# Kernel optimization log

Hardware: AMD Instinct MI355X
Metric: run time of the kernel (lower is better)

The kernel has to match this reference:

```python
import jax, jax.numpy as jnp
import numpy as np

B, S, D_MODEL, H = 2, 2048, 1024, 16
DIMS = D_MODEL // H  # 64


def setup_inputs() -> dict:
    key = jax.random.key(0)
    ks = jax.random.split(key, 7)
    scale = 1.0 / np.sqrt(D_MODEL)
    x = jax.random.normal(ks[0], (B, S, D_MODEL), dtype=jnp.float32)
    # Stacked per-head projection params: nn.Linear(d_model, dims) per head
    Wq = jax.random.uniform(ks[1], (H, DIMS, D_MODEL), minval=-scale, maxval=scale, dtype=jnp.float32)
    Wk = jax.random.uniform(ks[2], (H, DIMS, D_MODEL), minval=-scale, maxval=scale, dtype=jnp.float32)
    Wv = jax.random.uniform(ks[3], (H, DIMS, D_MODEL), minval=-scale, maxval=scale, dtype=jnp.float32)
    bq = jax.random.uniform(ks[4], (H, DIMS), minval=-scale, maxval=scale, dtype=jnp.float32)
    bk = jax.random.uniform(ks[5], (H, DIMS), minval=-scale, maxval=scale, dtype=jnp.float32)
    bv = jax.random.uniform(ks[6], (H, DIMS), minval=-scale, maxval=scale, dtype=jnp.float32)
    return {"x": x, "Wq": Wq, "Wk": Wk, "Wv": Wv, "bq": bq, "bk": bk, "bv": bv}


def reference(x, Wq, Wk, Wv, bq, bk, bv):
    # Per-head linear projections: [B,S,D] x [H,E,D] -> [B,H,S,E]
    q = jnp.einsum('bsd,hed->bhse', x, Wq) + bq[None, :, None, :]
    k = jnp.einsum('bsd,hed->bhse', x, Wk) + bk[None, :, None, :]
    v = jnp.einsum('bsd,hed->bhse', x, Wv) + bv[None, :, None, :]
    norm = DIMS ** (-0.5)
    # (q @ k^T) * norm @ v  -- NO softmax, as in the source
    scores = jnp.einsum('bhse,bhte->bhst', q, k) * norm  # [B,H,S,S]
    out = jnp.einsum('bhst,bhte->bhse', scores, v)       # [B,H,S,E]
    # concat heads along feature dim (head order matches torch.cat)
    return out.transpose(0, 2, 1, 3).reshape(B, S, H * DIMS)
```

## Files before the change

### kernel.cpp

```cpp
#include <hip/hip_runtime.h>


typedef __attribute__((ext_vector_type(8))) __bf16 bf16x8;
typedef __attribute__((ext_vector_type(8))) short short8;
typedef __attribute__((ext_vector_type(4))) float f32x4;
typedef __attribute__((ext_vector_type(4))) unsigned short ushort4v;

#define NX  4194304
#define NW1 1048576
#define NW  3145728

__device__ __forceinline__ float bf2f(unsigned short u) {
  union { unsigned int i; float f; } v; v.i = ((unsigned int)u) << 16; return v.f;
}
__device__ __forceinline__ unsigned short f2bf(float f) {
  union { float f; unsigned int i; } v; v.f = f;
  unsigned int u = v.i;
  u += 0x7fffu + ((u >> 16) & 1u);
  return (unsigned short)(u >> 16);
}

__global__ __launch_bounds__(256) void convert_pack(
    const float* __restrict__ x,
    const float* __restrict__ wq, const float* __restrict__ wk,
    const float* __restrict__ wv,
    const float* __restrict__ bq, const float* __restrict__ bk,
    const float* __restrict__ bv,
    unsigned short* __restrict__ Xbf, unsigned short* __restrict__ Wcat,
    float* __restrict__ Bcat)
{
  const long long t8 = ((long long)blockIdx.x * 256 + threadIdx.x) * 8;
  const float* src;
  unsigned short* dst;
  long long off;
  if (t8 < NX) {
    src = x; dst = Xbf; off = t8;
  } else if (t8 < NX + NW) {
    const long long w = t8 - NX;
    const int z = (int)(w >> 20);
    off = w & (NW1 - 1);
    src = (z == 0) ? wq : (z == 1) ? wk : wv;
    dst = Wcat + (long long)z * NW1;
  } else if (t8 < NX + NW + 3072) {
    const long long bo = t8 - (NX + NW);
    const int z = (int)(bo >> 10);
    const long long o2 = bo & 1023;
    const float* bsrc = (z == 0) ? bq : (z == 1) ? bk : bv;
    *(f32x4*)(Bcat + z * 1024 + o2)     = *(const f32x4*)(bsrc + o2);
    *(f32x4*)(Bcat + z * 1024 + o2 + 4) = *(const f32x4*)(bsrc + o2 + 4);
    return;
  } else {
    return;
  }
  f32x4 v0 = *(const f32x4*)(src + off);
  f32x4 v1 = *(const f32x4*)(src + off + 4);
  union { short8 s; unsigned short u[8]; } o;
#pragma unroll
  for (int j = 0; j < 4; ++j) {
    o.u[j]     = f2bf(v0[j]);
    o.u[4 + j] = f2bf(v1[j]);
  }
  *(short8*)(dst + off) = o.s;
}

#define ABUF_B 16384
#define TILE_B 28672
__global__ __launch_bounds__(512, 2) void qkv_gemm(
    const unsigned short* __restrict__ Xbf,
    const unsigned short* __restrict__ Wcat,
    const float* __restrict__ Bcat,
    unsigned short* __restrict__ Qt,
    unsigned short* __restrict__ Kt,
    unsigned short* __restrict__ Vt)
{
  __shared__ unsigned char lds[3 * TILE_B];

  const int tid = threadIdx.x;
  int bid = blockIdx.x;
  bid = (bid & 7) * 32 + (bid >> 3);
  const int colBase = (bid & 15) * 192;
  const int rowBase = (bid >> 4) * 256;

  const int lane = tid & 63;
  const int wid  = tid >> 6;
  const int wr = (wid >> 2) * 128;
  const int wc = (wid & 3) * 48;
  const int lr = lane & 15;
  const int lk = lane >> 4;
  const int fofs = (lk ^ ((lr >> 1) & 3)) << 4;

  const bool isA = (tid < 256);
  const int nload = isA ? 4 : 3;
  const int tloc = tid & 255;

  const unsigned short* gp[4];
  int lofs[4];
#pragma unroll
  for (int l = 0; l < 4; ++l) {
    const int unit = l * 256 + tloc;
    const int row  = unit >> 2;
    const int sc   = ((unit & 3) ^ ((row >> 1) & 3)) << 3;
    const int rowc = (!isA && row > 191) ? 0 : row;
    gp[l]  = isA ? (Xbf  + (size_t)(rowBase + rowc) * 1024 + sc)
                 : (Wcat + (size_t)(colBase + rowc) * 1024 + sc);
    lofs[l] = (isA ? 0 : ABUF_B) + unit * 16;
  }

  f32x4 acc[8][3] = {};
  short8 stg[3][4];

#pragma unroll
  for (int s = 0; s < 3; ++s)
#pragma unroll
    for (int l = 0; l < 4; ++l)
      if (l < nload) stg[s][l] = *(const short8*)(gp[l] + s * 32);
#pragma unroll
  for (int l = 0; l < 4; ++l)
    if (l < nload) *(short8*)(lds + lofs[l]) = stg[0][l];
  asm volatile("s_waitcnt lgkmcnt(0)" ::: "memory");

#define ITER(J, U, U1)                                                     \
  if ((J) < 32) {                                                          \
    __builtin_amdgcn_s_barrier();                                          \
    __builtin_amdgcn_sched_barrier(0);                                     \
    const unsigned char* Ab_ = lds + (U) * TILE_B;                         \
    const unsigned char* Bb_ = Ab_ + ABUF_B;                               \
    bf16x8 a_[8], b_[3];                                                   \
    _Pragma("unroll") for (int m = 0; m < 8; ++m)                          \
      a_[m] = *(const bf16x8*)(Ab_ + (wr + m * 16 + lr) * 64 + fofs);      \
    _Pragma("unroll") for (int n = 0; n < 3; ++n)                          \
      b_[n] = *(const bf16x8*)(Bb_ + (wc + n * 16 + lr) * 64 + fofs);      \
    if ((J) + 1 < 32) {                                                    \
      unsigned char* Wb_ = lds + (U1) * TILE_B;                            \
      _Pragma("unroll") for (int l = 0; l < 4; ++l)                        \
        if (l < nload) *(short8*)(Wb_ + lofs[l]) = stg[U1][l];             \
    }                                                                      \
    if ((J) + 3 < 32) {                                                    \
      _Pragma("unroll") for (int l = 0; l < 4; ++l)                        \
        if (l < nload) stg[U][l] = *(const short8*)(gp[l] + ((J) + 3) * 32);\
    }                                                                      \
    __builtin_amdgcn_s_setprio(1);                                         \
    _Pragma("unroll") for (int m = 0; m < 8; ++m)                          \
      _Pragma("unroll") for (int n = 0; n < 3; ++n)                        \
        acc[m][n] = __builtin_amdgcn_mfma_f32_16x16x32_bf16(               \
            a_[m], b_[n], acc[m][n], 0, 0, 0);                             \
    __builtin_amdgcn_s_setprio(0);                                         \
    asm volatile("s_waitcnt lgkmcnt(0)" ::: "memory");                     \
  }

  for (int jb = 0; jb < 32; jb += 3) {
    ITER(jb + 0, 0, 1);
    ITER(jb + 1, 1, 2);
    ITER(jb + 2, 2, 0);
  }
#undef ITER

  const int bB = rowBase >> 11;
#pragma unroll
  for (int n = 0; n < 3; ++n) {
    const int colG = colBase + wc + n * 16 + lr;
    const float bval = Bcat[colG];
    const int zone = colG >> 10;
    unsigned short* __restrict__ T = (zone == 0) ? Qt : (zone == 1) ? Kt : Vt;
    const int hf = (colG >> 6) & 15;
    const int f  = colG & 63;
    const size_t rowOff = ((size_t)(bB * 16 + hf) * 64 + f) * 2048;
#pragma unroll
    for (int m = 0; m < 8; ++m) {
      const int t = (rowBase + wr + m * 16 + lk * 4) & 2047;
      ushort4v pk;
#pragma unroll
      for (int jj = 0; jj < 4; ++jj)
        pk[jj] = f2bf(acc[m][n][jj] + bval);
      *(ushort4v*)&T[rowOff + t] = pk;
    }
  }
}

__global__ __launch_bounds__(64) void kv_outer(
    const unsigned short* __restrict__ Kt,
    const unsigned short* __restrict__ Vt,
    float* __restrict__ Mpart)
{
  const int lane = threadIdx.x;
  const int blk = blockIdx.x;
  const int bh = blk >> 3, tc = blk & 7;
  const int lr = lane & 15, lk = lane >> 4;
  const size_t base = (size_t)bh * 64 * 2048;

  f32x4 acc[4][4] = {};
#pragma unroll
  for (int ks = 0; ks < 8; ++ks) {
    const int t0 = tc * 256 + ks * 32 + lk * 8;
    bf16x8 af[4], bf[4];
#pragma unroll
    for (int m = 0; m < 4; ++m)
      af[m] = *(const bf16x8*)&Kt[base + (size_t)(m * 16 + lr) * 2048 + t0];
#pragma unroll
    for (int n = 0; n < 4; ++n)
      bf[n] = *(const bf16x8*)&Vt[base + (size_t)(n * 16 + lr) * 2048 + t0];
#pragma unroll
    for (int m = 0; m < 4; ++m)
#pragma unroll
      for (int n = 0; n < 4; ++n)
        acc[m][n] = __builtin_amdgcn_mfma_f32_16x16x32_bf16(af[m], bf[n], acc[m][n], 0, 0, 0);
  }
  float* out = Mpart + (size_t)blk * 4096;
#pragma unroll
  for (int m = 0; m < 4; ++m)
#pragma unroll
    for (int n = 0; n < 4; ++n)
#pragma unroll
      for (int j = 0; j < 4; ++j)
        out[(m * 16 + lk * 4 + j) * 64 + n * 16 + lr] = acc[m][n][j];
}

__global__ __launch_bounds__(256) void qm_out(
    const unsigned short* __restrict__ Qt, const float* __restrict__ Mpart,
    float* __restrict__ Out)
{
  __shared__ float Ms[64 * 64];
  __shared__ float Qst[64 * 132];
  const int tid = threadIdx.x;
  const int b = blockIdx.z, h = blockIdx.y, s0 = blockIdx.x * 128;
  const int bh = b * 16 + h;

#pragma unroll
  for (int i = 0; i < 4; ++i) {
    const int off = i * 1024 + tid * 4;
    f32x4 s = {};
#pragma unroll
    for (int ch = 0; ch < 8; ++ch)
      s += *(const f32x4*)&Mpart[((size_t)bh * 8 + ch) * 4096 + off];
    s *= 0.125f;
    *(f32x4*)&Ms[off] = s;
  }
  const size_t qbase = (size_t)bh * 64 * 2048;
#pragma unroll
  for (int i = 0; i < 4; ++i) {
    const int slot = i * 256 + tid;
    const int f = slot >> 4, c = slot & 15;
    short8 q = *(const short8*)&Qt[qbase + (size_t)f * 2048 + s0 + c * 8];
#pragma unroll
    for (int j = 0; j < 8; ++j)
      Qst[f * 132 + c * 8 + j] = bf2f((unsigned short)q[j]);
  }
  __syncthreads();

  const int s = (tid >> 3) * 4;
  const int e0 = (tid & 7) * 8;
  float acc2[4][8] = {};
  for (int f = 0; f < 64; ++f) {
    f32x4 m0 = *(const f32x4*)&Ms[f * 64 + e0];
    f32x4 m1 = *(const f32x4*)&Ms[f * 64 + e0 + 4];
#pragma unroll
    for (int i = 0; i < 4; ++i) {
      const float q = Qst[f * 132 + s + i];
#pragma unroll
      for (int j = 0; j < 4; ++j) {
        acc2[i][j]     += q * m0[j];
        acc2[i][j + 4] += q * m1[j];
      }
    }
  }
  const size_t obase = ((size_t)b * 2048 + s0) * 1024 + h * 64;
#pragma unroll
  for (int i = 0; i < 4; ++i) {
    f32x4 o0 = { acc2[i][0], acc2[i][1], acc2[i][2], acc2[i][3] };
    f32x4 o1 = { acc2[i][4], acc2[i][5], acc2[i][6], acc2[i][7] };
    *(f32x4*)&Out[obase + (size_t)(s + i) * 1024 + e0]     = o0;
    *(f32x4*)&Out[obase + (size_t)(s + i) * 1024 + e0 + 4] = o1;
  }
}

extern "C" void kernel_launch(void* const* d_in, const int* in_sizes, int n_in,
                              void* d_out, int out_size, void* d_ws, size_t ws_size,
                              hipStream_t stream) {
  const float* x  = (const float*)d_in[0];
  const float* Wq = (const float*)d_in[1];
  const float* Wk = (const float*)d_in[2];
  const float* Wv = (const float*)d_in[3];
  const float* bq = (const float*)d_in[4];
  const float* bk = (const float*)d_in[5];
  const float* bv = (const float*)d_in[6];
  float* out = (float*)d_out;

  char* ws = (char*)d_ws;
  const size_t MiB = 1024ull * 1024ull;
  unsigned short* Xbf   = (unsigned short*)(ws);
  unsigned short* Wcat  = (unsigned short*)(ws + 8  * MiB);
  float*          Bcat  = (float*)         (ws + 14 * MiB);
  unsigned short* Qt    = (unsigned short*)(ws + 15 * MiB);
  unsigned short* Kt    = (unsigned short*)(ws + 23 * MiB);
  unsigned short* Vt    = (unsigned short*)(ws + 31 * MiB);
  float*          Mpart = (float*)         (ws + 39 * MiB);

  convert_pack<<<3586, 256, 0, stream>>>(x, Wq, Wk, Wv, bq, bk, bv,
                                         Xbf, Wcat, Bcat);
  qkv_gemm<<<256, 512, 0, stream>>>(Xbf, Wcat, Bcat, Qt, Kt, Vt);
  kv_outer<<<256, 64, 0, stream>>>(Kt, Vt, Mpart);
  qm_out<<<dim3(16, 16, 2), 256, 0, stream>>>(Qt, Mpart, out);
}
```

Before: 67.05 us.

## Restructure QKV GEMM main loop to BK=64 double-buffered LDS with phased MFMA

The QKV projection GEMM changes from a triple-buffered BK=32 pipeline, where half the threads load A and half load B, to a double-buffered BK=64 pipeline. Every thread now issues both A and B global loads, using an 8-chunk XOR swizzle. Each k-step is split into three MFMA phases, with LDS fragment reads, global-load issue and LDS writes for the next buffer interleaved between barriers. The aim is to halve the number of loop iterations and barrier stalls and to overlap memory traffic with MFMA work. In exchange the kernel uses more LDS and registers, drops occupancy to one block per CU, and adds more barriers per iteration.

```diff
diff --git a/kernel.cpp b/kernel.cpp
--- a/kernel.cpp
+++ b/kernel.cpp
@@ -63,9 +63,11 @@
   *(short8*)(dst + off) = o.s;
 }
 
-#define ABUF_B 16384
-#define TILE_B 28672
-__global__ __launch_bounds__(512, 2) void qkv_gemm(
+#define ASEC 32768
+#define BUF_B 57344
+#define LGKM0 asm volatile("s_waitcnt lgkmcnt(0)" ::: "memory"); \
+              __builtin_amdgcn_sched_barrier(0)
+__global__ __launch_bounds__(512, 1) void qkv_gemm(
     const unsigned short* __restrict__ Xbf,
     const unsigned short* __restrict__ Wcat,
     const float* __restrict__ Bcat,
@@ -73,7 +75,7 @@
     unsigned short* __restrict__ Kt,
     unsigned short* __restrict__ Vt)
 {
-  __shared__ unsigned char lds[3 * TILE_B];
+  __shared__ unsigned char lds[2 * BUF_B];
 
   const int tid = threadIdx.x;
   int bid = blockIdx.x;
@@ -87,73 +89,104 @@
   const int wc = (wid & 3) * 48;
   const int lr = lane & 15;
   const int lk = lane >> 4;
-  const int fofs = (lk ^ ((lr >> 1) & 3)) << 4;
-
-  const bool isA = (tid < 256);
-  const int nload = isA ? 4 : 3;
-  const int tloc = tid & 255;
-
-  const unsigned short* gp[4];
-  int lofs[4];
+
+  const unsigned short* gpA[4];
+  const unsigned short* gpB[3];
+  int dwA[4], dwB[3];
 #pragma unroll
   for (int l = 0; l < 4; ++l) {
-    const int unit = l * 256 + tloc;
-    const int row  = unit >> 2;
-    const int sc   = ((unit & 3) ^ ((row >> 1) & 3)) << 3;
-    const int rowc = (!isA && row > 191) ? 0 : row;
-    gp[l]  = isA ? (Xbf  + (size_t)(rowBase + rowc) * 1024 + sc)
-                 : (Wcat + (size_t)(colBase + rowc) * 1024 + sc);
-    lofs[l] = (isA ? 0 : ABUF_B) + unit * 16;
+    const int u = l * 512 + tid, row = u >> 3, ch = u & 7;
+    gpA[l] = Xbf + (size_t)(rowBase + row) * 1024 + ch * 8;
+    dwA[l] = row * 128 + ((ch ^ (row & 7)) << 4);
+  }
+#pragma unroll
+  for (int l = 0; l < 3; ++l) {
+    const int u = l * 512 + tid, row = u >> 3, ch = u & 7;
+    gpB[l] = Wcat + (size_t)(colBase + row) * 1024 + ch * 8;
+    dwB[l] = ASEC + row * 128 + ((ch ^ (row & 7)) << 4);
   }
 
   f32x4 acc[8][3] = {};
-  short8 stg[3][4];
-
-#pragma unroll
-  for (int s = 0; s < 3; ++s)
-#pragma unroll
-    for (int l = 0; l < 4; ++l)
-      if (l < nload) stg[s][l] = *(const short8*)(gp[l] + s * 32);
-#pragma unroll
-  for (int l = 0; l < 4; ++l)
-    if (l < nload) *(short8*)(lds + lofs[l]) = stg[0][l];
-  asm volatile("s_waitcnt lgkmcnt(0)" ::: "memory");
-
-#define ITER(J, U, U1)                                                     \
-  if ((J) < 32) {                                                          \
-    __builtin_amdgcn_s_barrier();                                          \
-    __builtin_amdgcn_sched_barrier(0);                                     \
-    const unsigned char* Ab_ = lds + (U) * TILE_B;                         \
-    const unsigned char* Bb_ = Ab_ + ABUF_B;                               \
-    bf16x8 a_[8], b_[3];                                                   \
-    _Pragma("unroll") for (int m = 0; m < 8; ++m)                          \
-      a_[m] = *(const bf16x8*)(Ab_ + (wr + m * 16 + lr) * 64 + fofs);      \
-    _Pragma("unroll") for (int n = 0; n < 3; ++n)                          \
-      b_[n] = *(const bf16x8*)(Bb_ + (wc + n * 16 + lr) * 64 + fofs);      \
-    if ((J) + 1 < 32) {                                                    \
-      unsigned char* Wb_ = lds + (U1) * TILE_B;                            \
-      _Pragma("unroll") for (int l = 0; l < 4; ++l)                        \
-        if (l < nload) *(short8*)(Wb_ + lofs[l]) = stg[U1][l];             \
-    }                                                                      \
-    if ((J) + 3 < 32) {                                                    \
-      _Pragma("unroll") for (int l = 0; l < 4; ++l)                        \
-        if (l < nload) stg[U][l] = *(const short8*)(gp[l] + ((J) + 3) * 32);\
-    }                                                                      \
-    __builtin_amdgcn_s_setprio(1);                                         \
-    _Pragma("unroll") for (int m = 0; m < 8; ++m)                          \
-      _Pragma("unroll") for (int n = 0; n < 3; ++n)                        \
-        acc[m][n] = __builtin_amdgcn_mfma_f32_16x16x32_bf16(               \
-            a_[m], b_[n], acc[m][n], 0, 0, 0);                             \
-    __builtin_amdgcn_s_setprio(0);                                         \
-    asm volatile("s_waitcnt lgkmcnt(0)" ::: "memory");                     \
-  }
-
-  for (int jb = 0; jb < 32; jb += 3) {
-    ITER(jb + 0, 0, 1);
-    ITER(jb + 1, 1, 2);
-    ITER(jb + 2, 2, 0);
+  short8 grA[2][4], grB[2][3];
+
+#define GISSUE(S, kofs)                                        \
+  { _Pragma("unroll") for (int l = 0; l < 4; ++l)              \
+      grA[S][l] = *(const short8*)(gpA[l] + (kofs));           \
+    _Pragma("unroll") for (int l = 0; l < 3; ++l)              \
+      grB[S][l] = *(const short8*)(gpB[l] + (kofs)); }
+#define AFRAG(buf, m, ks)                                                 \
+  (*(const bf16x8*)((buf) + (wr + (m)*16 + lr) * 128 +                    \
+      ((((ks)*4 + lk) ^ ((wr + (m)*16 + lr) & 7)) << 4)))
+#define BFRAG(buf, n, ks)                                                 \
+  (*(const bf16x8*)((buf) + ASEC + (wc + (n)*16 + lr) * 128 +             \
+      ((((ks)*4 + lk) ^ ((wc + (n)*16 + lr) & 7)) << 4)))
+#define MF(m, n, A, Bv)                                                   \
+  acc[m][n] = __builtin_amdgcn_mfma_f32_16x16x32_bf16((A), (Bv), acc[m][n], 0, 0, 0)
+
+  GISSUE(0, 0);
+  GISSUE(1, 64);
+  asm volatile("s_waitcnt vmcnt(7)" ::: "memory");
+#pragma unroll
+  for (int l = 0; l < 4; ++l) *(short8*)(lds + dwA[l]) = grA[0][l];
+#pragma unroll
+  for (int l = 0; l < 3; ++l) *(short8*)(lds + dwB[l]) = grB[0][l];
+  LGKM0;
+  __builtin_amdgcn_s_barrier();
+
+#define ITER(t, U)                                                          \
+  {                                                                         \
+    const unsigned char* bc = lds + ((t) & 1) * BUF_B;                      \
+    unsigned char* bo = lds + (((t) + 1) & 1) * BUF_B;                      \
+    bf16x8 a0[8], a1[8], b[4];                                              \
+                                                                   \
+    _Pragma("unroll") for (int m = 0; m < 8; ++m) a0[m] = AFRAG(bc, m, 0);  \
+    b[0] = BFRAG(bc, 0, 0); b[1] = BFRAG(bc, 1, 0);                         \
+    if ((t) + 2 < 16) GISSUE(U, ((t) + 2) * 64);                            \
+    __builtin_amdgcn_s_barrier(); LGKM0;                                    \
+    __builtin_amdgcn_s_setprio(1);                                          \
+    _Pragma("unroll") for (int m = 0; m < 8; ++m) MF(m, 0, a0[m], b[0]);    \
+    _Pragma("unroll") for (int m = 0; m < 8; ++m) MF(m, 1, a0[m], b[1]);    \
+    __builtin_amdgcn_s_setprio(0);                                          \
+    __builtin_amdgcn_s_barrier();                                           \
+                                                                   \
+    b[2] = BFRAG(bc, 2, 0);                                                 \
+    _Pragma("unroll") for (int m = 0; m < 8; ++m) a1[m] = AFRAG(bc, m, 1);  \
+    b[3] = BFRAG(bc, 0, 1);                                                 \
+    if ((t) + 1 < 16) {                                                     \
+      if ((t) + 2 < 16) asm volatile("s_waitcnt vmcnt(7)" ::: "memory");    \
+      else              asm volatile("s_waitcnt vmcnt(0)" ::: "memory");    \
+      _Pragma("unroll") for (int l = 0; l < 4; ++l)                         \
+        *(short8*)(bo + dwA[l]) = grA[1 - (U)][l];                          \
+    }                                                                       \
+    __builtin_amdgcn_s_barrier(); LGKM0;                                    \
+    __builtin_amdgcn_s_setprio(1);                                          \
+    _Pragma("unroll") for (int m = 0; m < 8; ++m) MF(m, 2, a0[m], b[2]);    \
+    _Pragma("unroll") for (int m = 0; m < 8; ++m) MF(m, 0, a1[m], b[3]);    \
+    __builtin_amdgcn_s_setprio(0);                                          \
+    __builtin_amdgcn_s_barrier();                                           \
+                                                                   \
+    b[0] = BFRAG(bc, 1, 1); b[1] = BFRAG(bc, 2, 1);                         \
+    if ((t) + 1 < 16) {                                                     \
+      _Pragma("unroll") for (int l = 0; l < 3; ++l)                         \
+        *(short8*)(bo + dwB[l]) = grB[1 - (U)][l];                          \
+    }                                                                       \
+    __builtin_amdgcn_s_barrier(); LGKM0;                                    \
+    __builtin_amdgcn_s_setprio(1);                                          \
+    _Pragma("unroll") for (int m = 0; m < 8; ++m) MF(m, 1, a1[m], b[0]);    \
+    _Pragma("unroll") for (int m = 0; m < 8; ++m) MF(m, 2, a1[m], b[1]);    \
+    __builtin_amdgcn_s_setprio(0);                                          \
+    __builtin_amdgcn_s_barrier();                                           \
+  }
+
+  for (int tb = 0; tb < 16; tb += 2) {
+    ITER(tb, 0);
+    ITER(tb + 1, 1);
   }
 #undef ITER
+#undef GISSUE
+#undef AFRAG
+#undef BFRAG
+#undef MF
 
   const int bB = rowBase >> 11;
 #pragma unroll
@@ -167,12 +200,12 @@
     const size_t rowOff = ((size_t)(bB * 16 + hf) * 64 + f) * 2048;
 #pragma unroll
     for (int m = 0; m < 8; ++m) {
-      const int t = (rowBase + wr + m * 16 + lk * 4) & 2047;
+      const int tpos = (rowBase + wr + m * 16 + lk * 4) & 2047;
       ushort4v pk;
 #pragma unroll
       for (int jj = 0; jj < 4; ++jj)
         pk[jj] = f2bf(acc[m][n][jj] + bval);
-      *(ushort4v*)&T[rowOff + t] = pk;
+      *(ushort4v*)&T[rowOff + tpos] = pk;
     }
   }
 }
```

After: 99.69 us. 1.49x slower.
